# Kernel tuning notes

Hardware: AMD Instinct MI355X
Metric: run time of the kernel (lower is better)

## Reference

```python
import jax, jax.numpy as jnp
import numpy as np

HIDDEN = 2048
NUM_HEADS = 32
NUM_KV_HEADS = 8
GROUP = NUM_HEADS // NUM_KV_HEADS  # 4
HEAD_DIM = HIDDEN // NUM_HEADS     # 64
SEQ = 2048


def setup_inputs() -> dict:
    key = jax.random.key(0)
    ks = jax.random.split(key, 5)
    s = HIDDEN ** -0.5
    x = jax.random.normal(ks[0], (SEQ, HIDDEN), jnp.float32)
    q_proj = jax.random.normal(ks[1], (HIDDEN, HIDDEN), jnp.float32) * s
    k_proj = jax.random.normal(ks[2], (HIDDEN, HIDDEN // GROUP), jnp.float32) * s
    v_proj = jax.random.normal(ks[3], (HIDDEN, HIDDEN // GROUP), jnp.float32) * s
    o_proj = jax.random.normal(ks[4], (HIDDEN, HIDDEN), jnp.float32) * s
    # inv_freq = 1/rsqrt(10000**(i/d)) = sqrt(10000**(i/d)) per the original module
    inv_freq = jnp.sqrt(10000.0 ** (jnp.arange(0, HEAD_DIM, 2) / HEAD_DIM)).astype(jnp.float32)
    return {"x": x, "q_proj": q_proj, "k_proj": k_proj, "v_proj": v_proj,
            "o_proj": o_proj, "inv_freq": inv_freq}


def _rope(x, inv_freq):
    # x: [S, ..., HEAD_DIM]; rotation per the original (nonstandard) formula.
    orig_dtype = x.dtype
    x = x.astype(jnp.float32)
    seq = jnp.arange(x.shape[0])
    angles = seq[:, None] * jax.lax.stop_gradient(inv_freq)[None, :]  # [S, HEAD_DIM//2]
    bshape = (x.shape[0],) + (1,) * (x.ndim - 2) + (HEAD_DIM // 2,)
    sins = jnp.sin(angles).reshape(bshape)
    coss = jnp.cos(angles).reshape(bshape)
    half, odd = jnp.split(x, 2, axis=-1)
    out = jnp.concatenate([half * coss + odd * sins, half * sins - odd * coss], axis=-1)
    return out.astype(orig_dtype)


def reference(x, q_proj, k_proj, v_proj, o_proj, inv_freq):
    S = x.shape[0]
    q = (x @ q_proj).reshape(S, NUM_KV_HEADS, GROUP, HEAD_DIM)
    k = (x @ k_proj).reshape(S, NUM_KV_HEADS, HEAD_DIM)
    v = (x @ v_proj).reshape(S, NUM_KV_HEADS, HEAD_DIM)
    q = _rope(q, inv_freq)
    k = _rope(k, inv_freq)
    # scores: [a=S, b=S, h=kv_heads, g=group]
    scores = jnp.einsum('ahgd,bhd->abhg', q, k) / (HEAD_DIM ** 0.5)
    mask = jnp.tril(jnp.ones((S, S), dtype=jnp.bool_))[:, :, None, None]
    scores = jnp.where(mask, scores, -jnp.inf)
    attn = jax.nn.softmax(scores, axis=1)  # softmax over b (axis=-3)
    o = jnp.einsum('abhg,bhd->ahgd', attn, v).reshape(S, HIDDEN)
    return o @ o_proj
```

## Files before the change

kernel.cpp:

```cpp
#include <hip/hip_runtime.h>


typedef __bf16 bf16_t;
typedef __bf16 bf16x4 __attribute__((ext_vector_type(4)));
typedef __bf16 bf16x8 __attribute__((ext_vector_type(8)));
typedef float  f32x4  __attribute__((ext_vector_type(4)));
typedef short  s16x4  __attribute__((ext_vector_type(4)));

#define S_LEN   2048
#define HID     2048
#define NKV     8
#define NH      32
#define DHEAD   64
#define KVW     (NKV * DHEAD)

__device__ __align__(16) bf16_t g_xb [S_LEN * HID];
__device__ __align__(16) bf16_t g_wTq[HID * HID];
__device__ __align__(16) bf16_t g_wTk[KVW * HID];
__device__ __align__(16) bf16_t g_wTv[KVW * HID];
__device__ __align__(16) bf16_t g_wTo[HID * HID];
__device__ __align__(16) bf16_t g_q [S_LEN * HID];
__device__ __align__(16) bf16_t g_k [S_LEN * KVW];
__device__ __align__(16) bf16_t g_vT[KVW * S_LEN];
__device__ __align__(16) bf16_t g_om[S_LEN * HID];
__device__ float g_ropeC[S_LEN * 32];
__device__ float g_ropeS[S_LEN * 32];

static __device__ inline s16x4 bc4(bf16x4 v) { s16x4 r; __builtin_memcpy(&r, &v, 8); return r; }

__device__ __forceinline__ void gll16(void* lds, const void* g) {
    __builtin_amdgcn_global_load_lds(
        (const __attribute__((address_space(1))) void*)g,
        (__attribute__((address_space(3))) void*)lds,
        16, 0, 0);
}

__global__ __launch_bounds__(256)
void prep_kernel(const float* __restrict__ x,
                 const float* __restrict__ qw, const float* __restrict__ kw,
                 const float* __restrict__ vw, const float* __restrict__ ow,
                 const void* __restrict__ invf_raw) {
    __shared__ float tile[64][65];
    int b = blockIdx.x, t = threadIdx.x;

    if (b < 256) {
        int idx = b * 256 + t;
        int s = idx >> 5, j = idx & 31;
        float f;
        if (*(const unsigned*)invf_raw == 0x3F800000u) {
            f = ((const float*)invf_raw)[j];
        } else {
            unsigned u = ((unsigned)((const unsigned short*)invf_raw)[j]) << 16;
            __builtin_memcpy(&f, &u, 4);
        }
        float a32 = (float)s * f;
        double a = (double)a32;
        g_ropeC[idx] = (float)cos(a);
        g_ropeS[idx] = (float)sin(a);
        return;
    }
    if (b < 4352) {
        int idx = (b - 256) * 256 + t;
        float4 v = reinterpret_cast<const float4*>(x)[idx];
        bf16x4 o;
        o[0] = (bf16_t)v.x; o[1] = (bf16_t)v.y; o[2] = (bf16_t)v.z; o[3] = (bf16_t)v.w;
        *reinterpret_cast<bf16x4*>(&g_xb[(size_t)idx * 4]) = o;
        return;
    }
    const float* in; bf16_t* outp; int R, C, tb;
    if (b < 5376)      { in = qw; outp = g_wTq; R = HID; C = HID; tb = b - 4352; }
    else if (b < 5632) { in = kw; outp = g_wTk; R = HID; C = KVW; tb = b - 5376; }
    else if (b < 5888) { in = vw; outp = g_wTv; R = HID; C = KVW; tb = b - 5632; }
    else               { in = ow; outp = g_wTo; R = HID; C = HID; tb = b - 5888; }
    int xt = C >> 6;
    int c0 = (tb % xt) * 64, r0 = (tb / xt) * 64;

    int tx4 = t & 15, ty = t >> 4;
    #pragma unroll
    for (int r = ty; r < 64; r += 16) {
        float4 v = *reinterpret_cast<const float4*>(
            &in[(size_t)(r0 + r) * C + c0 + tx4 * 4]);
        tile[r][tx4 * 4 + 0] = v.x;
        tile[r][tx4 * 4 + 1] = v.y;
        tile[r][tx4 * 4 + 2] = v.z;
        tile[r][tx4 * 4 + 3] = v.w;
    }
    __syncthreads();

    int cc = t & 63, j0 = t >> 6;
    #pragma unroll
    for (int jj = 0; jj < 2; ++jj) {
        int j = j0 + jj * 4;
        bf16x8 o8;
        #pragma unroll
        for (int i = 0; i < 8; ++i)
            o8[i] = (bf16_t)tile[8 * j + i][cc];
        *reinterpret_cast<bf16x8*>(&outp[(size_t)(c0 + cc) * R + r0 + 8 * j]) = o8;
    }
}

__global__ __launch_bounds__(256)
void gemm_fused_kernel(float* __restrict__ Cf, int which) {
    __shared__ __align__(16) bf16_t As[2][128 * 64];
    __shared__ __align__(16) bf16_t Bs[2][64 * 64];

    int t    = threadIdx.x;
    int lane = t & 63, wid = t >> 6;
    int quad = lane >> 4, l15 = lane & 15;

    int ntn  = (which == 1) ? 32 : 48;
    int nwg  = ntn * 16;
    int orig = blockIdx.x;
    int qq   = nwg >> 3;
    int wg   = (orig & 7) * qq + (orig >> 3);
    int my   = wg / ntn, nx = wg - my * ntn;
    int m0   = my * 128;

    const bf16_t* A; const bf16_t* Bt; int n0;
    if (which == 1)      { A = g_om; Bt = g_wTo; n0 = nx * 64; }
    else {
        A = g_xb;
        if (nx < 32)      { Bt = g_wTq; n0 = nx * 64; }
        else if (nx < 40) { Bt = g_wTk; n0 = (nx - 32) * 64; }
        else              { Bt = g_wTv; n0 = (nx - 40) * 64; }
    }

    int crow = lane >> 3;
    int gseg = (lane & 7) ^ crow;
    int so   = l15 & 7;
    int wm   = wid * 32;

    f32x4 acc[2][4];
    #pragma unroll
    for (int im = 0; im < 2; ++im)
        #pragma unroll
        for (int in = 0; in < 4; ++in)
            #pragma unroll
            for (int r = 0; r < 4; ++r) acc[im][in][r] = 0.f;

    auto stage = [&](int buf, int kt) {
        #pragma unroll
        for (int c = 0; c < 4; ++c)
            gll16(&As[buf][(wid * 4 + c) * 512],
                  A  + (size_t)(m0 + (wid * 4 + c) * 8 + crow) * HID + kt + gseg * 8);
        #pragma unroll
        for (int c = 0; c < 2; ++c)
            gll16(&Bs[buf][(wid * 2 + c) * 512],
                  Bt + (size_t)(n0 + (wid * 2 + c) * 8 + crow) * HID + kt + gseg * 8);
    };

    stage(0, 0);

    for (int it = 0; it < 32; ++it) {
        int cur = it & 1;
        if (it + 1 < 32) {
            stage(cur ^ 1, (it + 1) * 64);
            asm volatile("s_waitcnt vmcnt(6)" ::: "memory");
        } else {
            asm volatile("s_waitcnt vmcnt(0)" ::: "memory");
        }
        asm volatile("s_barrier" ::: "memory");

        #pragma unroll
        for (int kh = 0; kh < 2; ++kh) {
            bf16x8 af[2], bfv[4];
            #pragma unroll
            for (int i = 0; i < 2; ++i)
                af[i]  = *reinterpret_cast<const bf16x8*>(
                    &As[cur][(wm + i * 16 + l15) * 64 + (((kh * 4 + quad) ^ so) * 8)]);
            #pragma unroll
            for (int i = 0; i < 4; ++i)
                bfv[i] = *reinterpret_cast<const bf16x8*>(
                    &Bs[cur][(i * 16 + l15) * 64 + (((kh * 4 + quad) ^ so) * 8)]);
            #pragma unroll
            for (int im = 0; im < 2; ++im)
                #pragma unroll
                for (int in = 0; in < 4; ++in)
                    acc[im][in] = __builtin_amdgcn_mfma_f32_16x16x32_bf16(
                        af[im], bfv[in], acc[im][in], 0, 0, 0);
        }

        asm volatile("s_barrier" ::: "memory");
    }

    if (which == 1) {
        #pragma unroll
        for (int im = 0; im < 2; ++im) {
            int rowb = m0 + wm + im * 16 + quad * 4;
            #pragma unroll
            for (int in = 0; in < 4; ++in) {
                int col = n0 + in * 16 + l15;
                #pragma unroll
                for (int r = 0; r < 4; ++r)
                    Cf[(size_t)(rowb + r) * HID + col] = acc[im][in][r];
            }
        }
    } else if (nx < 40) {
        bf16_t* Cb; int N, colbase;
        if (nx < 32) { Cb = g_q; N = HID; colbase = nx * 64; }
        else         { Cb = g_k; N = KVW; colbase = (nx - 32) * 64; }
        #pragma unroll
        for (int im = 0; im < 2; ++im) {
            #pragma unroll
            for (int r = 0; r < 4; ++r) {
                int row = m0 + wm + im * 16 + quad * 4 + r;
                #pragma unroll
                for (int in = 0; in < 2; ++in) {
                    int d = in * 16 + l15;
                    float a  = acc[im][in][r];
                    float bb = acc[im][in + 2][r];
                    float cc = g_ropeC[row * 32 + d];
                    float ss = g_ropeS[row * 32 + d];
                    Cb[(size_t)row * N + colbase + d]      = (bf16_t)(a * cc + bb * ss);
                    Cb[(size_t)row * N + colbase + 32 + d] = (bf16_t)(a * ss - bb * cc);
                }
            }
        }
    } else {
        #pragma unroll
        for (int im = 0; im < 2; ++im) {
            int rowb = m0 + wm + im * 16 + quad * 4;
            #pragma unroll
            for (int in = 0; in < 4; ++in) {
                int col = (nx - 40) * 64 + in * 16 + l15;
                #pragma unroll
                for (int r = 0; r < 4; ++r)
                    g_vT[(size_t)col * S_LEN + (rowb + r)] = (bf16_t)acc[im][in][r];
            }
        }
    }
}

__global__ __launch_bounds__(512)
void flash_part_kernel() {
    __shared__ __align__(16) bf16_t SM[2][2][2][64 * 64];

    int t    = threadIdx.x;
    int lane = t & 63, wid = t >> 6;
    int g    = wid >> 2;
    int wh   = wid & 3;
    int quad = lane >> 4, l15 = lane & 15;
    int bx   = blockIdx.x;
    int hk   = bx & 7;
    int slot = bx >> 3;
    int qb32 = (slot < 32) ? slot : (95 - slot);
    int nkt  = (qb32 >> 1) + 1;
    int ng   = (nkt + 1) >> 1;

    int head = hk * 4 + wh;
    int q0   = qb32 * 32;

    int crow = lane >> 3;
    int gseg = (lane & 7) ^ crow;
    int so   = l15 & 7;

    bf16x8 aq[2][2];
    #pragma unroll
    for (int mq = 0; mq < 2; ++mq) {
        const bf16_t* qp = g_q + (size_t)(q0 + mq * 16 + l15) * HID + head * 64 + quad * 8;
        aq[mq][0] = *reinterpret_cast<const bf16x8*>(qp);
        aq[mq][1] = *reinterpret_cast<const bf16x8*>(qp + 32);
        #pragma unroll
        for (int j = 0; j < 8; ++j) {
            aq[mq][0][j] = (bf16_t)((float)aq[mq][0][j] * 0.125f);
            aq[mq][1][j] = (bf16_t)((float)aq[mq][1][j] * 0.125f);
        }
    }

    bf16x4 ones4;
    #pragma unroll
    for (int j = 0; j < 4; ++j) ones4[j] = (bf16_t)1.0f;
    s16x4 ones_s = bc4(ones4);

    f32x4 oacc[2][4], liacc[2];
    #pragma unroll
    for (int mq = 0; mq < 2; ++mq) {
        #pragma unroll
        for (int r = 0; r < 4; ++r) liacc[mq][r] = 0.f;
        #pragma unroll
        for (int dt = 0; dt < 4; ++dt)
            #pragma unroll
            for (int r = 0; r < 4; ++r) oacc[mq][dt][r] = 0.f;
    }

    int qcol[2] = { q0 + l15, q0 + 16 + l15 };

    auto stageKV = [&](int buf, int k0) {
        #pragma unroll
        for (int c = 0; c < 2; ++c) {
            int ch = wh * 2 + c;
            gll16(&SM[g][0][buf][ch * 512],
                  g_k  + (size_t)(k0 + ch * 8 + crow) * KVW + hk * 64 + gseg * 8);
            gll16(&SM[g][1][buf][ch * 512],
                  g_vT + (size_t)(hk * 64 + ch * 8 + crow) * S_LEN + k0 + gseg * 8);
        }
    };

    if (g < nkt) stageKV(0, g * 64);

    for (int i = 0; i < ng; ++i) {
        int cur  = i & 1;
        int kt   = 2 * i + g;
        bool live = (kt < nkt);
        int ktn  = kt + 2;
        bool stage_next = (i + 1 < ng) && (ktn < nkt);
        if (stage_next) {
            stageKV(cur ^ 1, ktn * 64);
            asm volatile("s_waitcnt vmcnt(4)" ::: "memory");
        } else {
            asm volatile("s_waitcnt vmcnt(0)" ::: "memory");
        }
        asm volatile("s_barrier" ::: "memory");

        if (live) {
            int k0 = kt * 64;
            bf16x8 ak[4][2];
            #pragma unroll
            for (int mk = 0; mk < 4; ++mk) {
                int row = mk * 16 + l15;
                ak[mk][0] = *reinterpret_cast<const bf16x8*>(&SM[g][0][cur][row * 64 + ((quad ^ so) * 8)]);
                ak[mk][1] = *reinterpret_cast<const bf16x8*>(&SM[g][0][cur][row * 64 + (((4 + quad) ^ so) * 8)]);
            }

            f32x4 sacc[4][2];
            #pragma unroll
            for (int mk = 0; mk < 4; ++mk)
                #pragma unroll
                for (int mq = 0; mq < 2; ++mq) {
                    f32x4 s;
                    #pragma unroll
                    for (int r = 0; r < 4; ++r) s[r] = 0.f;
                    s = __builtin_amdgcn_mfma_f32_16x16x32_bf16(ak[mk][0], aq[mq][0], s, 0, 0, 0);
                    s = __builtin_amdgcn_mfma_f32_16x16x32_bf16(ak[mk][1], aq[mq][1], s, 0, 0, 0);
                    sacc[mk][mq] = s;
                }

            s16x4 pas[4][2];
            #pragma unroll
            for (int mk = 0; mk < 4; ++mk)
                #pragma unroll
                for (int mq = 0; mq < 2; ++mq) {
                    bf16x4 pa;
                    #pragma unroll
                    for (int r = 0; r < 4; ++r) {
                        int kk = k0 + mk * 16 + quad * 4 + r;
                        pa[r] = (bf16_t)((kk <= qcol[mq]) ? __expf(sacc[mk][mq][r] - 16.0f) : 0.0f);
                    }
                    pas[mk][mq] = bc4(pa);
                }

            #pragma unroll
            for (int mk = 0; mk < 4; ++mk) {
                #pragma unroll
                for (int dt = 0; dt < 4; ++dt) {
                    int rv = dt * 16 + l15;
                    int vb = rv * 64 + (((mk * 2 + (quad >> 1)) ^ so) * 8) + (quad & 1) * 4;
                    bf16x4 bv = *reinterpret_cast<const bf16x4*>(&SM[g][1][cur][vb]);
                    s16x4 bvs = bc4(bv);
                    #pragma unroll
                    for (int mq = 0; mq < 2; ++mq)
                        oacc[mq][dt] = __builtin_amdgcn_mfma_f32_16x16x16bf16_1k(pas[mk][mq], bvs, oacc[mq][dt], 0, 0, 0);
                }
                #pragma unroll
                for (int mq = 0; mq < 2; ++mq)
                    liacc[mq] = __builtin_amdgcn_mfma_f32_16x16x16bf16_1k(pas[mk][mq], ones_s, liacc[mq], 0, 0, 0);
            }
        }

        asm volatile("s_barrier" ::: "memory");
    }

    float* pO = reinterpret_cast<float*>(&SM[1][0][0][0]);
    float* pl = reinterpret_cast<float*>(&SM[0][0][0][0]);
    if (g == 1) {
        #pragma unroll
        for (int mq = 0; mq < 2; ++mq)
            #pragma unroll
            for (int r = 0; r < 4; ++r) {
                int row = mq * 16 + quad * 4 + r;
                int sw  = ((row >> 2) & 3) << 3;
                #pragma unroll
                for (int dt = 0; dt < 4; ++dt)
                    pO[(wh * 32 + row) * 64 + ((dt * 16 + l15) ^ sw)] = oacc[mq][dt][r];
                if (l15 == 0) pl[wh * 32 + row] = liacc[mq][r];
            }
    }
    asm volatile("s_waitcnt lgkmcnt(0)" ::: "memory");
    asm volatile("s_barrier" ::: "memory");
    if (g == 0) {
        #pragma unroll
        for (int mq = 0; mq < 2; ++mq)
            #pragma unroll
            for (int r = 0; r < 4; ++r) {
                int row = mq * 16 + quad * 4 + r;
                int sw  = ((row >> 2) & 3) << 3;
                float l = liacc[mq][r] + pl[wh * 32 + row];
                float inv = 1.0f / l;
                #pragma unroll
                for (int dt = 0; dt < 4; ++dt) {
                    float o = oacc[mq][dt][r] + pO[(wh * 32 + row) * 64 + ((dt * 16 + l15) ^ sw)];
                    g_om[(size_t)(q0 + row) * HID + head * 64 + dt * 16 + l15] = (bf16_t)(o * inv);
                }
            }
    }
}

extern "C" void kernel_launch(void* const* d_in, const int* in_sizes, int n_in,
                              void* d_out, int out_size, void* d_ws, size_t ws_size,
                              hipStream_t stream) {
    const float* x    = (const float*)d_in[0];
    const float* qpW  = (const float*)d_in[1];
    const float* kpW  = (const float*)d_in[2];
    const float* vpW  = (const float*)d_in[3];
    const float* opW  = (const float*)d_in[4];
    const void*  invf = d_in[5];
    float* out = (float*)d_out;

    prep_kernel<<<6912, 256, 0, stream>>>(x, qpW, kpW, vpW, opW, invf);
    gemm_fused_kernel<<<768, 256, 0, stream>>>(nullptr, 0);
    flash_part_kernel<<<512, 512, 0, stream>>>();
    gemm_fused_kernel<<<512, 256, 0, stream>>>(out, 1);
}
```

Before: 229.7 us.

## Split GEMM kernels, use 64x64 tiles for O-proj, skip mask on interior tiles

The double-precision cos/sin in the RoPE table is replaced with single-precision cosf/sinf. The fused GEMM is split into a QKV-specialized kernel and a new 64x64-tile output-projection kernel launched with 1024 blocks. This gives the O-proj GEMM more workgroups across the CUs, at the cost of less data reuse per tile. In flash attention the causal mask compare is applied only on the last (diagonal) key tile, which removes per-element selects from interior tiles.

```diff
diff --git a/kernel.cpp b/kernel.cpp
--- a/kernel.cpp
+++ b/kernel.cpp
@@ -54,9 +54,8 @@
             __builtin_memcpy(&f, &u, 4);
         }
         float a32 = (float)s * f;
-        double a = (double)a32;
-        g_ropeC[idx] = (float)cos(a);
-        g_ropeS[idx] = (float)sin(a);
+        g_ropeC[idx] = cosf(a32);
+        g_ropeS[idx] = sinf(a32);
         return;
     }
     if (b < 4352) {
@@ -100,7 +99,7 @@
 }
 
 __global__ __launch_bounds__(256)
-void gemm_fused_kernel(float* __restrict__ Cf, int which) {
+void gemm_qkv_kernel() {
     __shared__ __align__(16) bf16_t As[2][128 * 64];
     __shared__ __align__(16) bf16_t Bs[2][64 * 64];
 
@@ -108,22 +107,16 @@
     int lane = t & 63, wid = t >> 6;
     int quad = lane >> 4, l15 = lane & 15;
 
-    int ntn  = (which == 1) ? 32 : 48;
-    int nwg  = ntn * 16;
     int orig = blockIdx.x;
-    int qq   = nwg >> 3;
-    int wg   = (orig & 7) * qq + (orig >> 3);
-    int my   = wg / ntn, nx = wg - my * ntn;
+    int wg   = (orig & 7) * 96 + (orig >> 3);
+    int my   = wg / 48, nx = wg - my * 48;
     int m0   = my * 128;
 
-    const bf16_t* A; const bf16_t* Bt; int n0;
-    if (which == 1)      { A = g_om; Bt = g_wTo; n0 = nx * 64; }
-    else {
-        A = g_xb;
-        if (nx < 32)      { Bt = g_wTq; n0 = nx * 64; }
-        else if (nx < 40) { Bt = g_wTk; n0 = (nx - 32) * 64; }
-        else              { Bt = g_wTv; n0 = (nx - 40) * 64; }
-    }
+    const bf16_t* Bt; int n0;
+    if (nx < 32)      { Bt = g_wTq; n0 = nx * 64; }
+    else if (nx < 40) { Bt = g_wTk; n0 = (nx - 32) * 64; }
+    else              { Bt = g_wTv; n0 = (nx - 40) * 64; }
+    const bf16_t* A = g_xb;
 
     int crow = lane >> 3;
     int gseg = (lane & 7) ^ crow;
@@ -183,19 +176,7 @@
         asm volatile("s_barrier" ::: "memory");
     }
 
-    if (which == 1) {
-        #pragma unroll
-        for (int im = 0; im < 2; ++im) {
-            int rowb = m0 + wm + im * 16 + quad * 4;
-            #pragma unroll
-            for (int in = 0; in < 4; ++in) {
-                int col = n0 + in * 16 + l15;
-                #pragma unroll
-                for (int r = 0; r < 4; ++r)
-                    Cf[(size_t)(rowb + r) * HID + col] = acc[im][in][r];
-            }
-        }
-    } else if (nx < 40) {
+    if (nx < 40) {
         bf16_t* Cb; int N, colbase;
         if (nx < 32) { Cb = g_q; N = HID; colbase = nx * 64; }
         else         { Cb = g_k; N = KVW; colbase = (nx - 32) * 64; }
@@ -227,6 +208,92 @@
                 for (int r = 0; r < 4; ++r)
                     g_vT[(size_t)col * S_LEN + (rowb + r)] = (bf16_t)acc[im][in][r];
             }
+        }
+    }
+}
+
+__global__ __launch_bounds__(256)
+void gemm_o64_kernel(float* __restrict__ Cf) {
+    __shared__ __align__(16) bf16_t As[2][64 * 64];
+    __shared__ __align__(16) bf16_t Bs[2][64 * 64];
+
+    int t    = threadIdx.x;
+    int lane = t & 63, wid = t >> 6;
+    int quad = lane >> 4, l15 = lane & 15;
+
+    int orig = blockIdx.x;
+    int wg   = (orig & 7) * 128 + (orig >> 3);
+    int my   = wg >> 5, nx = wg & 31;
+    int m0   = my * 64, n0 = nx * 64;
+
+    int crow = lane >> 3;
+    int gseg = (lane & 7) ^ crow;
+    int so   = l15 & 7;
+    int wr   = (wid >> 1) * 32;
+    int wc   = (wid & 1) * 32;
+
+    f32x4 acc[2][2];
+    #pragma unroll
+    for (int im = 0; im < 2; ++im)
+        #pragma unroll
+        for (int in = 0; in < 2; ++in)
+            #pragma unroll
+            for (int r = 0; r < 4; ++r) acc[im][in][r] = 0.f;
+
+    auto stage = [&](int buf, int kt) {
+        #pragma unroll
+        for (int c = 0; c < 2; ++c) {
+            int ch = wid * 2 + c;
+            gll16(&As[buf][ch * 512],
+                  g_om  + (size_t)(m0 + ch * 8 + crow) * HID + kt + gseg * 8);
+            gll16(&Bs[buf][ch * 512],
+                  g_wTo + (size_t)(n0 + ch * 8 + crow) * HID + kt + gseg * 8);
+        }
+    };
+
+    stage(0, 0);
+
+    for (int it = 0; it < 32; ++it) {
+        int cur = it & 1;
+        if (it + 1 < 32) {
+            stage(cur ^ 1, (it + 1) * 64);
+            asm volatile("s_waitcnt vmcnt(4)" ::: "memory");
+        } else {
+            asm volatile("s_waitcnt vmcnt(0)" ::: "memory");
+        }
+        asm volatile("s_barrier" ::: "memory");
+
+        #pragma unroll
+        for (int kh = 0; kh < 2; ++kh) {
+            bf16x8 af[2], bfv[2];
+            #pragma unroll
+            for (int im = 0; im < 2; ++im)
+                af[im]  = *reinterpret_cast<const bf16x8*>(
+                    &As[cur][(wr + im * 16 + l15) * 64 + (((kh * 4 + quad) ^ so) * 8)]);
+            #pragma unroll
+            for (int in = 0; in < 2; ++in)
+                bfv[in] = *reinterpret_cast<const bf16x8*>(
+                    &Bs[cur][(wc + in * 16 + l15) * 64 + (((kh * 4 + quad) ^ so) * 8)]);
+            #pragma unroll
+            for (int im = 0; im < 2; ++im)
+                #pragma unroll
+                for (int in = 0; in < 2; ++in)
+                    acc[im][in] = __builtin_amdgcn_mfma_f32_16x16x32_bf16(
+                        af[im], bfv[in], acc[im][in], 0, 0, 0);
+        }
+
+        asm volatile("s_barrier" ::: "memory");
+    }
+
+    #pragma unroll
+    for (int im = 0; im < 2; ++im) {
+        int rowb = m0 + wr + im * 16 + quad * 4;
+        #pragma unroll
+        for (int in = 0; in < 2; ++in) {
+            int col = n0 + wc + in * 16 + l15;
+            #pragma unroll
+            for (int r = 0; r < 4; ++r)
+                Cf[(size_t)(rowb + r) * HID + col] = acc[im][in][r];
         }
     }
 }
@@ -336,18 +403,31 @@
                 }
 
             s16x4 pas[4][2];
-            #pragma unroll
-            for (int mk = 0; mk < 4; ++mk)
-                #pragma unroll
-                for (int mq = 0; mq < 2; ++mq) {
-                    bf16x4 pa;
+            if (kt == nkt - 1) {
+                #pragma unroll
+                for (int mk = 0; mk < 4; ++mk)
                     #pragma unroll
-                    for (int r = 0; r < 4; ++r) {
-                        int kk = k0 + mk * 16 + quad * 4 + r;
-                        pa[r] = (bf16_t)((kk <= qcol[mq]) ? __expf(sacc[mk][mq][r] - 16.0f) : 0.0f);
+                    for (int mq = 0; mq < 2; ++mq) {
+                        bf16x4 pa;
+                        #pragma unroll
+                        for (int r = 0; r < 4; ++r) {
+                            int kk = k0 + mk * 16 + quad * 4 + r;
+                            pa[r] = (bf16_t)((kk <= qcol[mq]) ? __expf(sacc[mk][mq][r] - 16.0f) : 0.0f);
+                        }
+                        pas[mk][mq] = bc4(pa);
                     }
-                    pas[mk][mq] = bc4(pa);
-                }
+            } else {
+                #pragma unroll
+                for (int mk = 0; mk < 4; ++mk)
+                    #pragma unroll
+                    for (int mq = 0; mq < 2; ++mq) {
+                        bf16x4 pa;
+                        #pragma unroll
+                        for (int r = 0; r < 4; ++r)
+                            pa[r] = (bf16_t)__expf(sacc[mk][mq][r] - 16.0f);
+                        pas[mk][mq] = bc4(pa);
+                    }
+            }
 
             #pragma unroll
             for (int mk = 0; mk < 4; ++mk) {
@@ -417,7 +497,7 @@
     float* out = (float*)d_out;
 
     prep_kernel<<<6912, 256, 0, stream>>>(x, qpW, kpW, vpW, opW, invf);
-    gemm_fused_kernel<<<768, 256, 0, stream>>>(nullptr, 0);
+    gemm_qkv_kernel<<<768, 256, 0, stream>>>();
     flash_part_kernel<<<512, 512, 0, stream>>>();
-    gemm_fused_kernel<<<512, 256, 0, stream>>>(out, 1);
+    gemm_o64_kernel<<<1024, 256, 0, stream>>>(out);
 }
```

Result: no change. 231.7 us (+0.9%).

## Move o_proj transpose into QKV GEMM launch, use float trig, skip mask off-diagonal

Applied to the files above, without the earlier changes.

The o_proj weight transpose/convert now runs as 1024 extra blocks appended to the QKV GEMM launch instead of in the prep kernel, so it can fill idle CUs during the GEMM tail. The rope table now uses single-precision cosf/sinf instead of double cos/sin. In the flash kernel the causal mask comparison is applied only on the last (diagonal) key tile, and earlier tiles skip the per-element compare. The float trig may lose accuracy at large angles, and the extra GEMM blocks may compete with the GEMM tiles for CUs.

```diff
diff --git a/kernel.cpp b/kernel.cpp
--- a/kernel.cpp
+++ b/kernel.cpp
@@ -38,7 +38,7 @@
 __global__ __launch_bounds__(256)
 void prep_kernel(const float* __restrict__ x,
                  const float* __restrict__ qw, const float* __restrict__ kw,
-                 const float* __restrict__ vw, const float* __restrict__ ow,
+                 const float* __restrict__ vw,
                  const void* __restrict__ invf_raw) {
     __shared__ float tile[64][65];
     int b = blockIdx.x, t = threadIdx.x;
@@ -54,9 +54,8 @@
             __builtin_memcpy(&f, &u, 4);
         }
         float a32 = (float)s * f;
-        double a = (double)a32;
-        g_ropeC[idx] = (float)cos(a);
-        g_ropeS[idx] = (float)sin(a);
+        g_ropeC[idx] = cosf(a32);
+        g_ropeS[idx] = sinf(a32);
         return;
     }
     if (b < 4352) {
@@ -70,8 +69,7 @@
     const float* in; bf16_t* outp; int R, C, tb;
     if (b < 5376)      { in = qw; outp = g_wTq; R = HID; C = HID; tb = b - 4352; }
     else if (b < 5632) { in = kw; outp = g_wTk; R = HID; C = KVW; tb = b - 5376; }
-    else if (b < 5888) { in = vw; outp = g_wTv; R = HID; C = KVW; tb = b - 5632; }
-    else               { in = ow; outp = g_wTo; R = HID; C = HID; tb = b - 5888; }
+    else               { in = vw; outp = g_wTv; R = HID; C = KVW; tb = b - 5632; }
     int xt = C >> 6;
     int c0 = (tb % xt) * 64, r0 = (tb / xt) * 64;
 
@@ -100,11 +98,41 @@
 }
 
 __global__ __launch_bounds__(256)
-void gemm_fused_kernel(float* __restrict__ Cf, int which) {
+void gemm_fused_kernel(float* __restrict__ Cf, int which,
+                       const float* __restrict__ ow) {
     __shared__ __align__(16) bf16_t As[2][128 * 64];
     __shared__ __align__(16) bf16_t Bs[2][64 * 64];
 
     int t    = threadIdx.x;
+
+    if (which == 0 && blockIdx.x >= 768) {
+        float (*tile)[65] = reinterpret_cast<float (*)[65]>(&As[0][0]);
+        int tb = blockIdx.x - 768;
+        int c0 = (tb & 31) * 64, r0 = (tb >> 5) * 64;
+        int tx4 = t & 15, ty = t >> 4;
+        #pragma unroll
+        for (int r = ty; r < 64; r += 16) {
+            float4 v = *reinterpret_cast<const float4*>(
+                &ow[(size_t)(r0 + r) * HID + c0 + tx4 * 4]);
+            tile[r][tx4 * 4 + 0] = v.x;
+            tile[r][tx4 * 4 + 1] = v.y;
+            tile[r][tx4 * 4 + 2] = v.z;
+            tile[r][tx4 * 4 + 3] = v.w;
+        }
+        __syncthreads();
+        int cc = t & 63, j0 = t >> 6;
+        #pragma unroll
+        for (int jj = 0; jj < 2; ++jj) {
+            int j = j0 + jj * 4;
+            bf16x8 o8;
+            #pragma unroll
+            for (int i = 0; i < 8; ++i)
+                o8[i] = (bf16_t)tile[8 * j + i][cc];
+            *reinterpret_cast<bf16x8*>(&g_wTo[(size_t)(c0 + cc) * HID + r0 + 8 * j]) = o8;
+        }
+        return;
+    }
+
     int lane = t & 63, wid = t >> 6;
     int quad = lane >> 4, l15 = lane & 15;
 
@@ -336,18 +364,31 @@
                 }
 
             s16x4 pas[4][2];
-            #pragma unroll
-            for (int mk = 0; mk < 4; ++mk)
-                #pragma unroll
-                for (int mq = 0; mq < 2; ++mq) {
-                    bf16x4 pa;
+            if (kt == nkt - 1) {
+                #pragma unroll
+                for (int mk = 0; mk < 4; ++mk)
                     #pragma unroll
-                    for (int r = 0; r < 4; ++r) {
-                        int kk = k0 + mk * 16 + quad * 4 + r;
-                        pa[r] = (bf16_t)((kk <= qcol[mq]) ? __expf(sacc[mk][mq][r] - 16.0f) : 0.0f);
+                    for (int mq = 0; mq < 2; ++mq) {
+                        bf16x4 pa;
+                        #pragma unroll
+                        for (int r = 0; r < 4; ++r) {
+                            int kk = k0 + mk * 16 + quad * 4 + r;
+                            pa[r] = (bf16_t)((kk <= qcol[mq]) ? __expf(sacc[mk][mq][r] - 16.0f) : 0.0f);
+                        }
+                        pas[mk][mq] = bc4(pa);
                     }
-                    pas[mk][mq] = bc4(pa);
-                }
+            } else {
+                #pragma unroll
+                for (int mk = 0; mk < 4; ++mk)
+                    #pragma unroll
+                    for (int mq = 0; mq < 2; ++mq) {
+                        bf16x4 pa;
+                        #pragma unroll
+                        for (int r = 0; r < 4; ++r)
+                            pa[r] = (bf16_t)__expf(sacc[mk][mq][r] - 16.0f);
+                        pas[mk][mq] = bc4(pa);
+                    }
+            }
 
             #pragma unroll
             for (int mk = 0; mk < 4; ++mk) {
@@ -416,8 +457,8 @@
     const void*  invf = d_in[5];
     float* out = (float*)d_out;
 
-    prep_kernel<<<6912, 256, 0, stream>>>(x, qpW, kpW, vpW, opW, invf);
-    gemm_fused_kernel<<<768, 256, 0, stream>>>(nullptr, 0);
+    prep_kernel<<<5888, 256, 0, stream>>>(x, qpW, kpW, vpW, invf);
+    gemm_fused_kernel<<<1792, 256, 0, stream>>>(nullptr, 0, opW);
     flash_part_kernel<<<512, 512, 0, stream>>>();
-    gemm_fused_kernel<<<512, 256, 0, stream>>>(out, 1);
+    gemm_fused_kernel<<<512, 256, 0, stream>>>(out, 1, nullptr);
 }
```

New measurement: 228.5 us. Within noise of the previous version (-0.5%).
